# Kernel tuning notes

Hardware: AMD Instinct MI355X
Metric: run time of the kernel (lower is better)

Reference implementation:

```python
import jax, jax.numpy as jnp
import numpy as np

EMB = 768
HEADS = 8
HEAD_DIM = EMB // HEADS
SCALE = HEAD_DIM ** -0.5


def setup_inputs() -> dict:
    key = jax.random.key(0)
    ks = jax.random.split(key, 9)
    s = 0.02
    return {
        "x": jax.random.normal(ks[0], (2, 4096, EMB), dtype=jnp.float32),
        "Wq": jax.random.normal(ks[1], (EMB, EMB), dtype=jnp.float32) * s,
        "bq": jax.random.normal(ks[2], (EMB,), dtype=jnp.float32) * s,
        "Wk": jax.random.normal(ks[3], (EMB, EMB), dtype=jnp.float32) * s,
        "bk": jax.random.normal(ks[4], (EMB,), dtype=jnp.float32) * s,
        "Wv": jax.random.normal(ks[5], (EMB, EMB), dtype=jnp.float32) * s,
        "bv": jax.random.normal(ks[6], (EMB,), dtype=jnp.float32) * s,
        "Wo": jax.random.normal(ks[7], (EMB, EMB), dtype=jnp.float32) * s,
        "bo": jax.random.normal(ks[8], (EMB,), dtype=jnp.float32) * s,
    }


def reference(x, Wq, bq, Wk, bk, Wv, bv, Wo, bo):
    b, n, _ = x.shape
    # torch Linear: y = x @ W.T + b
    def split_heads(y):  # [b, n, emb] -> [b, h, n, d]
        return y.reshape(b, n, HEADS, HEAD_DIM).transpose(0, 2, 1, 3)

    q = split_heads(x @ Wq.T + bq)
    k = split_heads(x @ Wk.T + bk)
    v = split_heads(x @ Wv.T + bv)
    # scores [b, h, q, k]; source applies scaling inside softmax input
    scores = jnp.einsum('bhqd,bhkd->bhqk', q, k) * SCALE
    weight = jax.nn.softmax(scores, axis=-1)
    out = jnp.einsum('bhqk,bhkd->bhqd', weight, v)
    out = out.transpose(0, 2, 1, 3).reshape(b, n, EMB)
    return out @ Wo.T + bo
```

## Files before the change

### kernel.cpp

```cpp
#include <hip/hip_runtime.h>


typedef __bf16 bf16;
typedef __attribute__((ext_vector_type(2))) float f32x2;
typedef __attribute__((ext_vector_type(4))) float f32x4;
typedef __attribute__((ext_vector_type(16))) float f32x16;
typedef __attribute__((ext_vector_type(8))) __bf16 bf16x8;
typedef __attribute__((ext_vector_type(4))) __bf16 bf16x4;
typedef __attribute__((ext_vector_type(4))) unsigned u32x4;

#define EMB 768
#define SEQ 4096
#define NB 2
#define NHEADS 8
#define HD 96
#define BHTOT (NB * NHEADS)
#define MTOT (NB * SEQ)
#define QSCALE 0.14724241052735512f

#define AS1 __attribute__((address_space(1)))
#define AS3 __attribute__((address_space(3)))

__global__ __launch_bounds__(256) void cast_f32_bf16(const float* __restrict__ in,
                                                     bf16* __restrict__ out) {
  const int i = (blockIdx.x * 256 + threadIdx.x) * 4;
  const f32x4 v = *reinterpret_cast<const f32x4*>(in + i);
  bf16x4 o;
  o[0] = (bf16)v[0]; o[1] = (bf16)v[1]; o[2] = (bf16)v[2]; o[3] = (bf16)v[3];
  *reinterpret_cast<bf16x4*>(out + i) = o;
}

__global__ __launch_bounds__(256) void cast_w4(const float* __restrict__ w0,
                                               const float* __restrict__ w1,
                                               const float* __restrict__ w2,
                                               const float* __restrict__ w3,
                                               bf16* __restrict__ o0,
                                               bf16* __restrict__ o1,
                                               bf16* __restrict__ o2,
                                               bf16* __restrict__ o3) {
  const float* w = (blockIdx.y == 0) ? w0 : (blockIdx.y == 1) ? w1 : (blockIdx.y == 2) ? w2 : w3;
  bf16* o = (blockIdx.y == 0) ? o0 : (blockIdx.y == 1) ? o1 : (blockIdx.y == 2) ? o2 : o3;
  const int i = (blockIdx.x * 256 + threadIdx.x) * 4;
  const f32x4 v = *reinterpret_cast<const f32x4*>(w + i);
  bf16x4 ob;
  ob[0] = (bf16)v[0]; ob[1] = (bf16)v[1]; ob[2] = (bf16)v[2]; ob[3] = (bf16)v[3];
  *reinterpret_cast<bf16x4*>(o + i) = ob;
}

template <int MODE>
__global__ __launch_bounds__(256) void gemm_bt(const bf16* __restrict__ A,
                                               const bf16* __restrict__ B,
                                               const float* __restrict__ b0,
                                               const float* __restrict__ b1,
                                               const float* __restrict__ b2,
                                               void* __restrict__ out,
                                               void* __restrict__ outK) {
  constexpr int K = EMB;
  __shared__ bf16 As[128 * 32];
  __shared__ bf16 Bs[128 * 32];
  const int tid = threadIdx.x;
  const int lane = tid & 63;
  const int wid = tid >> 6;
  const int wr = wid >> 1, wc = wid & 1;
  const int l15 = lane & 15, l4 = lane >> 4;
  const int rowBase = blockIdx.y * 128;
  const int colBase = blockIdx.x * 128;

  f32x4 acc[4][4] = {};

  for (int kt = 0; kt < K / 32; ++kt) {
    const int kb = kt * 32;
#pragma unroll
    for (int i = 0; i < 2; ++i) {
      const int c = (wid * 2 + i) * 64 + lane;
      const int row = c >> 2, cc = c & 3;
      const bf16* ga = A + (size_t)(rowBase + row) * K + kb + cc * 8;
      const bf16* gb = B + (size_t)(colBase + row) * K + kb + cc * 8;
      __builtin_amdgcn_global_load_lds(
          (const AS1 void*)ga,
          (AS3 void*)(As + (size_t)(wid * 2 + i) * 512), 16, 0, 0);
      __builtin_amdgcn_global_load_lds(
          (const AS1 void*)gb,
          (AS3 void*)(Bs + (size_t)(wid * 2 + i) * 512), 16, 0, 0);
    }
    __syncthreads();
    bf16x8 af[4], bfr[4];
#pragma unroll
    for (int t = 0; t < 4; ++t) {
      af[t]  = *reinterpret_cast<const bf16x8*>(As + (wr * 64 + t * 16 + l15) * 32 + l4 * 8);
      bfr[t] = *reinterpret_cast<const bf16x8*>(Bs + (wc * 64 + t * 16 + l15) * 32 + l4 * 8);
    }
#pragma unroll
    for (int mt = 0; mt < 4; ++mt)
#pragma unroll
      for (int nt = 0; nt < 4; ++nt)
        acc[mt][nt] = __builtin_amdgcn_mfma_f32_16x16x32_bf16(af[mt], bfr[nt], acc[mt][nt], 0, 0, 0);
    __syncthreads();
  }

#pragma unroll
  for (int mt = 0; mt < 4; ++mt) {
#pragma unroll
    for (int nt = 0; nt < 4; ++nt) {
      const int gn = colBase + wc * 64 + nt * 16 + l15;
      if (MODE == 0) {
        const int mm = gn / 768;
        const int g7 = gn - mm * 768;
        const int h = g7 / HD, d = g7 - h * HD;
        const float* bp = (mm == 0) ? b0 : (mm == 1) ? b1 : b2;
        const float bv = bp[g7];
        const float sc = (mm == 0) ? QSCALE : 1.f;
#pragma unroll
        for (int r = 0; r < 4; ++r) {
          const int gm = rowBase + wr * 64 + mt * 16 + l4 * 4 + r;
          const int b = gm >> 12, n = gm & (SEQ - 1);
          const float v = (acc[mt][nt][r] + bv) * sc;
          if (mm == 1) {
            ((bf16*)outK)[((size_t)(b * NHEADS + h) * SEQ + n) * 128 +
                          (((d >> 3) ^ (n & 7)) << 3) + (d & 7)] = (bf16)v;
          } else {
            bf16* dst = (bf16*)out + (mm == 2 ? (size_t)MTOT * EMB : 0);
            dst[((size_t)(b * NHEADS + h) * SEQ + n) * HD + d] = (bf16)v;
          }
        }
      } else {
        const float bv = b0[gn];
#pragma unroll
        for (int r = 0; r < 4; ++r) {
          const int gm = rowBase + wr * 64 + mt * 16 + l4 * 4 + r;
          ((float*)out)[(size_t)gm * EMB + gn] = acc[mt][nt][r] + bv;
        }
      }
    }
  }
}

__global__ __launch_bounds__(256) void transpose_v(const bf16* __restrict__ v,
                                                   bf16* __restrict__ vt) {
  __shared__ bf16 T[96][72];
  const int bh = blockIdx.y;
  const int n0 = blockIdx.x * 64;
  const int tid = threadIdx.x;
#pragma unroll
  for (int i = 0; i < 3; ++i) {
    const int c = i * 256 + tid;
    const int n = c / 12, cc = c % 12;
    const bf16x8 val = *reinterpret_cast<const bf16x8*>(
        v + ((size_t)bh * SEQ + n0 + n) * HD + cc * 8);
#pragma unroll
    for (int j = 0; j < 8; ++j) T[cc * 8 + j][n] = val[j];
  }
  __syncthreads();
#pragma unroll
  for (int i = 0; i < 3; ++i) {
    const int c = i * 256 + tid;
    const int d = c >> 3, nc = c & 7;
    const int s0i = (nc >> 1) * 16 + (nc & 1) * 4;
    const bf16x4 lo = *reinterpret_cast<const bf16x4*>(&T[d][s0i]);
    const bf16x4 hi = *reinterpret_cast<const bf16x4*>(&T[d][s0i + 8]);
    const bf16x8 val = __builtin_shufflevector(lo, hi, 0, 1, 2, 3, 4, 5, 6, 7);
    const int pc = nc ^ (d & 7);
    *reinterpret_cast<bf16x8*>(vt + ((size_t)bh * HD + d) * SEQ + n0 + pc * 8) = val;
  }
}

template <int SPLIT>
__global__ __launch_bounds__(256, 2) void attn_fwd(const bf16* __restrict__ q,
                                                   const bf16* __restrict__ ksw,
                                                   const bf16* __restrict__ vt,
                                                   void* __restrict__ outp,
                                                   float* __restrict__ lsum) {
  __shared__ bf16 Ks[2][64 * 128];
  __shared__ bf16 Vts[2][96 * 64];
  const int tid = threadIdx.x;
  const int lane = tid & 63;
  const int wid = tid >> 6;
  const int l31 = lane & 31, lhi = lane >> 5;
  const int lin = (blockIdx.z * gridDim.y + blockIdx.y) * gridDim.x + blockIdx.x;
  const int nblk = 256 * SPLIT;
  const int cpx = nblk >> 3;
  const int l2 = (lin & 7) * cpx + (lin >> 3);
  const int qblk = l2 & 15;
  const int z = (SPLIT == 2) ? ((l2 >> 4) & 1) : 0;
  const int bh = (SPLIT == 2) ? (l2 >> 5) : (l2 >> 4);
  const int q0 = qblk * 256 + wid * 64;
  constexpr int NT = SEQ / 64 / SPLIT;
  const int kv00 = z * NT * 64;
  const size_t headq = (size_t)bh * SEQ * HD;
  const bf16* kg = ksw + (size_t)bh * SEQ * 128;
  const bf16* vg = vt + (size_t)bh * (size_t)HD * SEQ;

  const bf16* kp = kg + (size_t)kv00 * 128 + (size_t)tid * 8;
  const bf16* vp = vg + (size_t)(tid >> 3) * SEQ + kv00 + (tid & 7) * 8;

  int krd[12], vrd[12];
#pragma unroll
  for (int kib = 0; kib < 2; ++kib)
#pragma unroll
    for (int dc = 0; dc < 6; ++dc) {
      const int row = kib * 32 + l31;
      krd[kib * 6 + dc] = (row * 128 + (((dc * 2 + lhi) ^ (l31 & 7)) * 8)) * 2;
    }
#pragma unroll
  for (int db = 0; db < 3; ++db)
#pragma unroll
    for (int kb = 0; kb < 4; ++kb) {
      const int row = db * 32 + l31;
      vrd[db * 4 + kb] = (row * 64 + (((kb * 2 + lhi) ^ (l31 & 7)) * 8)) * 2;
    }

  bf16x8 qf[2][6];
#pragma unroll
  for (int g = 0; g < 2; ++g)
#pragma unroll
    for (int dc = 0; dc < 6; ++dc)
      qf[g][dc] = *reinterpret_cast<const bf16x8*>(
          q + headq + (size_t)(q0 + g * 32 + l31) * HD + dc * 16 + lhi * 8);

  f32x16 oacc[2][3] = {};
  float lrun[2] = {0.f, 0.f};

#pragma unroll
  for (int i = 0; i < 4; ++i)
    __builtin_amdgcn_global_load_lds((const AS1 void*)(kp + i * 2048),
                                     (AS3 void*)(&Ks[0][i * 2048 + tid * 8]), 16, 0, 0);
#pragma unroll
  for (int i = 0; i < 3; ++i)
    __builtin_amdgcn_global_load_lds((const AS1 void*)(vp + (size_t)i * 32 * SEQ),
                                     (AS3 void*)(&Vts[0][i * 2048 + tid * 8]), 16, 0, 0);
  kp += 8192;
  vp += 64;
  __syncthreads();

  for (int kt = 0; kt < NT; ++kt) {
    const int cur = kt & 1;
    if (kt < NT - 1) {
#pragma unroll
      for (int i = 0; i < 4; ++i)
        __builtin_amdgcn_global_load_lds((const AS1 void*)(kp + i * 2048),
                                         (AS3 void*)(&Ks[cur ^ 1][i * 2048 + tid * 8]), 16, 0, 0);
#pragma unroll
      for (int i = 0; i < 3; ++i)
        __builtin_amdgcn_global_load_lds((const AS1 void*)(vp + (size_t)i * 32 * SEQ),
                                         (AS3 void*)(&Vts[cur ^ 1][i * 2048 + tid * 8]), 16, 0, 0);
      kp += 8192;
      vp += 64;
    }
    const char* ksb = (const char*)Ks[cur];
    const char* vsb = (const char*)Vts[cur];

    bf16x8 pf[2][4];
#pragma unroll
    for (int kib = 0; kib < 2; ++kib) {
      f32x16 s[2] = {};
      __builtin_amdgcn_s_setprio(1);
#pragma unroll
      for (int dc = 0; dc < 6; ++dc) {
        const bf16x8 kf = *reinterpret_cast<const bf16x8*>(ksb + krd[kib * 6 + dc]);
        s[0] = __builtin_amdgcn_mfma_f32_32x32x16_bf16(kf, qf[0][dc], s[0], 0, 0, 0);
        s[1] = __builtin_amdgcn_mfma_f32_32x32x16_bf16(kf, qf[1][dc], s[1], 0, 0, 0);
      }
      __builtin_amdgcn_s_setprio(0);
#pragma unroll
      for (int g = 0; g < 2; ++g) {
        float a0 = 0.f, a1 = 0.f, a2 = 0.f, a3 = 0.f;
#pragma unroll
        for (int i = 0; i < 4; ++i) {
          s[g][4 * i + 0] = __builtin_amdgcn_exp2f(s[g][4 * i + 0]); a0 += s[g][4 * i + 0];
          s[g][4 * i + 1] = __builtin_amdgcn_exp2f(s[g][4 * i + 1]); a1 += s[g][4 * i + 1];
          s[g][4 * i + 2] = __builtin_amdgcn_exp2f(s[g][4 * i + 2]); a2 += s[g][4 * i + 2];
          s[g][4 * i + 3] = __builtin_amdgcn_exp2f(s[g][4 * i + 3]); a3 += s[g][4 * i + 3];
        }
        lrun[g] += (a0 + a1) + (a2 + a3);
        unsigned c[8];
#pragma unroll
        for (int i = 0; i < 8; ++i)
          asm("v_cvt_pk_bf16_f32 %0, %1, %2"
              : "=v"(c[i]) : "v"(s[g][2 * i]), "v"(s[g][2 * i + 1]));
        const u32x4 wa = {c[0], c[1], c[2], c[3]};
        const u32x4 wb = {c[4], c[5], c[6], c[7]};
        pf[g][kib * 2 + 0] = __builtin_bit_cast(bf16x8, wa);
        pf[g][kib * 2 + 1] = __builtin_bit_cast(bf16x8, wb);
      }
    }

    __builtin_amdgcn_s_setprio(1);
#pragma unroll
    for (int kb = 0; kb < 4; ++kb) {
#pragma unroll
      for (int db = 0; db < 3; ++db) {
        const bf16x8 vf = *reinterpret_cast<const bf16x8*>(vsb + vrd[db * 4 + kb]);
        oacc[0][db] = __builtin_amdgcn_mfma_f32_32x32x16_bf16(vf, pf[0][kb], oacc[0][db], 0, 0, 0);
        oacc[1][db] = __builtin_amdgcn_mfma_f32_32x32x16_bf16(vf, pf[1][kb], oacc[1][db], 0, 0, 0);
      }
    }
    __builtin_amdgcn_s_setprio(0);

    __syncthreads();
  }

  const int b = bh >> 3, h = bh & 7;
#pragma unroll
  for (int g = 0; g < 2; ++g) {
    float lr = lrun[g];
    lr += __shfl_xor(lr, 32, 64);
    const int n = q0 + g * 32 + l31;
    if (SPLIT == 2) {
      float* po = (float*)outp + (size_t)z * ((size_t)BHTOT * SEQ * HD) +
                  ((size_t)bh * SEQ + n) * HD;
#pragma unroll
      for (int db = 0; db < 3; ++db)
#pragma unroll
        for (int i = 0; i < 8; ++i) {
          const int r = 2 * i;
          const int d = db * 32 + (r & 3) + 8 * (r >> 2) + 4 * lhi;
          f32x2 w = {oacc[g][db][r], oacc[g][db][r + 1]};
          *reinterpret_cast<f32x2*>(po + d) = w;
        }
      if (lhi == 0) lsum[(size_t)z * BHTOT * SEQ + (size_t)bh * SEQ + n] = lr;
    } else {
      const float inv = 1.f / lr;
      bf16* obase = (bf16*)outp + (size_t)(b * SEQ + n) * EMB + h * HD;
#pragma unroll
      for (int db = 0; db < 3; ++db)
#pragma unroll
        for (int i = 0; i < 8; ++i) {
          const int r = 2 * i;
          const int d = db * 32 + (r & 3) + 8 * (r >> 2) + 4 * lhi;
          unsigned w;
          const float v0 = oacc[g][db][r] * inv, v1 = oacc[g][db][r + 1] * inv;
          asm("v_cvt_pk_bf16_f32 %0, %1, %2" : "=v"(w) : "v"(v0), "v"(v1));
          *reinterpret_cast<unsigned*>(obase + d) = w;
        }
    }
  }
}

__global__ __launch_bounds__(256) void merge_o(const float* __restrict__ p,
                                               const float* __restrict__ ls,
                                               bf16* __restrict__ ao) {
  const int idx = blockIdx.x * 256 + threadIdx.x;
  const size_t PS = (size_t)BHTOT * SEQ * HD;
  const f32x4 a = *reinterpret_cast<const f32x4*>(p + (size_t)idx * 4);
  const f32x4 b2 = *reinterpret_cast<const f32x4*>(p + PS + (size_t)idx * 4);
  const int rest = idx / 24;
  const int d4 = idx - rest * 24;
  const float inv = 1.f / (ls[rest] + ls[BHTOT * SEQ + rest]);
  const int bh = rest >> 12, n = rest & (SEQ - 1);
  const int b = bh >> 3, h = bh & 7;
  bf16x4 o4;
#pragma unroll
  for (int j = 0; j < 4; ++j) o4[j] = (bf16)((a[j] + b2[j]) * inv);
  *reinterpret_cast<bf16x4*>(ao + (size_t)(b * SEQ + n) * EMB + h * HD + d4 * 4) = o4;
}

extern "C" void kernel_launch(void* const* d_in, const int* in_sizes, int n_in,
                              void* d_out, int out_size, void* d_ws, size_t ws_size,
                              hipStream_t stream) {
  const float* x  = (const float*)d_in[0];
  const float* Wq = (const float*)d_in[1];
  const float* bq = (const float*)d_in[2];
  const float* Wk = (const float*)d_in[3];
  const float* bk = (const float*)d_in[4];
  const float* Wv = (const float*)d_in[5];
  const float* bv = (const float*)d_in[6];
  const float* Wo = (const float*)d_in[7];
  const float* bo = (const float*)d_in[8];

  const size_t XN = (size_t)MTOT * EMB;
  const size_t WN = (size_t)EMB * EMB;
  const size_t KSWN = (size_t)BHTOT * SEQ * 128;

  bf16* p = (bf16*)d_ws;
  bf16* xbf  = p; p += XN;
  bf16* wqb  = p; p += WN;
  bf16* wkb  = p; p += WN;
  bf16* wvb  = p; p += WN;
  bf16* wob  = p; p += WN;
  bf16* qb   = p; p += XN;
  bf16* vb   = p; p += XN;
  bf16* kbsw = p; p += KSWN;
  bf16* vtb  = p; p += XN;
  bf16* ao   = p; p += XN;
  const size_t base_bytes = (size_t)((char*)p - (char*)d_ws);
  float* part = (float*)p;
  float* lsum = part + 2 * ((size_t)BHTOT * SEQ * HD);
  const size_t need2 = base_bytes + (2 * (size_t)BHTOT * SEQ * HD) * 4 +
                       (2 * (size_t)BHTOT * SEQ) * 4;
  const bool split2 = (ws_size >= need2);

  cast_f32_bf16<<<XN / 1024, 256, 0, stream>>>(x, xbf);
  cast_w4<<<dim3(WN / 1024, 4), 256, 0, stream>>>(Wq, Wk, Wv, Wo, wqb, wkb, wvb, wob);

  gemm_bt<0><<<dim3(3 * EMB / 128, MTOT / 128), 256, 0, stream>>>(
      xbf, wqb, bq, bk, bv, qb, kbsw);

  transpose_v<<<dim3(SEQ / 64, BHTOT), 256, 0, stream>>>(vb, vtb);

  if (split2) {
    attn_fwd<2><<<dim3(16, 16, 2), 256, 0, stream>>>(qb, kbsw, vtb, part, lsum);
    merge_o<<<(BHTOT * SEQ * HD / 4) / 256, 256, 0, stream>>>(part, lsum, ao);
  } else {
    attn_fwd<1><<<dim3(16, 16, 1), 256, 0, stream>>>(qb, kbsw, vtb, ao, nullptr);
  }

  gemm_bt<1><<<dim3(EMB / 128, MTOT / 128), 256, 0, stream>>>(
      ao, wob, bo, nullptr, nullptr, d_out, nullptr);
}
```

Measured before the change: 211.0 us.

## Halve attention query tile, compact unpadded K layout, bf16 split partials

```diff
diff --git a/kernel.cpp b/kernel.cpp
--- a/kernel.cpp
+++ b/kernel.cpp
@@ -2,7 +2,6 @@
 
 
 typedef __bf16 bf16;
-typedef __attribute__((ext_vector_type(2))) float f32x2;
 typedef __attribute__((ext_vector_type(4))) float f32x4;
 typedef __attribute__((ext_vector_type(16))) float f32x16;
 typedef __attribute__((ext_vector_type(8))) __bf16 bf16x8;
@@ -17,6 +16,7 @@
 #define BHTOT (NB * NHEADS)
 #define MTOT (NB * SEQ)
 #define QSCALE 0.14724241052735512f
+#define KIMG_BH (SEQ * 96)
 
 #define AS1 __attribute__((address_space(1)))
 #define AS3 __attribute__((address_space(3)))
@@ -116,8 +116,10 @@
           const int b = gm >> 12, n = gm & (SEQ - 1);
           const float v = (acc[mt][nt][r] + bv) * sc;
           if (mm == 1) {
-            ((bf16*)outK)[((size_t)(b * NHEADS + h) * SEQ + n) * 128 +
-                          (((d >> 3) ^ (n & 7)) << 3) + (d & 7)] = (bf16)v;
+            ((bf16*)outK)[(size_t)(b * NHEADS + h) * KIMG_BH +
+                          (size_t)(n >> 6) * 6144 + (d >> 5) * 2048 +
+                          (n & 63) * 32 +
+                          ((((d >> 3) & 3) ^ ((n >> 1) & 3)) << 3) + (d & 7)] = (bf16)v;
           } else {
             bf16* dst = (bf16*)out + (mm == 2 ? (size_t)MTOT * EMB : 0);
             dst[((size_t)(b * NHEADS + h) * SEQ + n) * HD + d] = (bf16)v;
@@ -165,32 +167,32 @@
 }
 
 template <int SPLIT>
-__global__ __launch_bounds__(256, 2) void attn_fwd(const bf16* __restrict__ q,
-                                                   const bf16* __restrict__ ksw,
+__global__ __launch_bounds__(256, 3) void attn_fwd(const bf16* __restrict__ q,
+                                                   const bf16* __restrict__ kimg,
                                                    const bf16* __restrict__ vt,
                                                    void* __restrict__ outp,
                                                    float* __restrict__ lsum) {
-  __shared__ bf16 Ks[2][64 * 128];
+  __shared__ bf16 Ks[2][3 * 2048];
   __shared__ bf16 Vts[2][96 * 64];
   const int tid = threadIdx.x;
   const int lane = tid & 63;
   const int wid = tid >> 6;
   const int l31 = lane & 31, lhi = lane >> 5;
   const int lin = (blockIdx.z * gridDim.y + blockIdx.y) * gridDim.x + blockIdx.x;
-  const int nblk = 256 * SPLIT;
-  const int cpx = nblk >> 3;
-  const int l2 = (lin & 7) * cpx + (lin >> 3);
-  const int qblk = l2 & 15;
-  const int z = (SPLIT == 2) ? ((l2 >> 4) & 1) : 0;
-  const int bh = (SPLIT == 2) ? (l2 >> 5) : (l2 >> 4);
-  const int q0 = qblk * 256 + wid * 64;
+  constexpr int NBLK = 512 * SPLIT;
+  constexpr int CPX = NBLK >> 3;
+  const int l2 = (lin & 7) * CPX + (lin >> 3);
+  const int qblk = l2 & 31;
+  const int z = (SPLIT == 2) ? ((l2 >> 5) & 1) : 0;
+  const int bh = (SPLIT == 2) ? (l2 >> 6) : (l2 >> 5);
+  const int q0 = qblk * 128 + wid * 32;
   constexpr int NT = SEQ / 64 / SPLIT;
   const int kv00 = z * NT * 64;
   const size_t headq = (size_t)bh * SEQ * HD;
-  const bf16* kg = ksw + (size_t)bh * SEQ * 128;
+  const bf16* kg = kimg + (size_t)bh * KIMG_BH;
   const bf16* vg = vt + (size_t)bh * (size_t)HD * SEQ;
 
-  const bf16* kp = kg + (size_t)kv00 * 128 + (size_t)tid * 8;
+  const bf16* kp = kg + (size_t)(kv00 >> 6) * 6144 + (size_t)tid * 8;
   const bf16* vp = vg + (size_t)(tid >> 3) * SEQ + kv00 + (tid & 7) * 8;
 
   int krd[12], vrd[12];
@@ -198,8 +200,10 @@
   for (int kib = 0; kib < 2; ++kib)
 #pragma unroll
     for (int dc = 0; dc < 6; ++dc) {
+      const int j = dc * 2 + lhi;
       const int row = kib * 32 + l31;
-      krd[kib * 6 + dc] = (row * 128 + (((dc * 2 + lhi) ^ (l31 & 7)) * 8)) * 2;
+      krd[kib * 6 + dc] =
+          ((j >> 2) * 2048 + row * 32 + (((j & 3) ^ ((l31 >> 1) & 3)) << 3)) * 2;
     }
 #pragma unroll
   for (int db = 0; db < 3; ++db)
@@ -209,26 +213,23 @@
       vrd[db * 4 + kb] = (row * 64 + (((kb * 2 + lhi) ^ (l31 & 7)) * 8)) * 2;
     }
 
-  bf16x8 qf[2][6];
-#pragma unroll
-  for (int g = 0; g < 2; ++g)
-#pragma unroll
-    for (int dc = 0; dc < 6; ++dc)
-      qf[g][dc] = *reinterpret_cast<const bf16x8*>(
-          q + headq + (size_t)(q0 + g * 32 + l31) * HD + dc * 16 + lhi * 8);
-
-  f32x16 oacc[2][3] = {};
-  float lrun[2] = {0.f, 0.f};
-
-#pragma unroll
-  for (int i = 0; i < 4; ++i)
+  bf16x8 qf[6];
+#pragma unroll
+  for (int dc = 0; dc < 6; ++dc)
+    qf[dc] = *reinterpret_cast<const bf16x8*>(
+        q + headq + (size_t)(q0 + l31) * HD + dc * 16 + lhi * 8);
+
+  f32x16 oacc[3] = {};
+  float lrun = 0.f;
+
+#pragma unroll
+  for (int i = 0; i < 3; ++i) {
     __builtin_amdgcn_global_load_lds((const AS1 void*)(kp + i * 2048),
                                      (AS3 void*)(&Ks[0][i * 2048 + tid * 8]), 16, 0, 0);
-#pragma unroll
-  for (int i = 0; i < 3; ++i)
     __builtin_amdgcn_global_load_lds((const AS1 void*)(vp + (size_t)i * 32 * SEQ),
                                      (AS3 void*)(&Vts[0][i * 2048 + tid * 8]), 16, 0, 0);
-  kp += 8192;
+  }
+  kp += 6144;
   vp += 64;
   __syncthreads();
 
@@ -236,52 +237,59 @@
     const int cur = kt & 1;
     if (kt < NT - 1) {
 #pragma unroll
-      for (int i = 0; i < 4; ++i)
+      for (int i = 0; i < 3; ++i) {
         __builtin_amdgcn_global_load_lds((const AS1 void*)(kp + i * 2048),
                                          (AS3 void*)(&Ks[cur ^ 1][i * 2048 + tid * 8]), 16, 0, 0);
-#pragma unroll
-      for (int i = 0; i < 3; ++i)
         __builtin_amdgcn_global_load_lds((const AS1 void*)(vp + (size_t)i * 32 * SEQ),
                                          (AS3 void*)(&Vts[cur ^ 1][i * 2048 + tid * 8]), 16, 0, 0);
-      kp += 8192;
+      }
+      kp += 6144;
       vp += 64;
     }
     const char* ksb = (const char*)Ks[cur];
     const char* vsb = (const char*)Vts[cur];
 
-    bf16x8 pf[2][4];
-#pragma unroll
-    for (int kib = 0; kib < 2; ++kib) {
-      f32x16 s[2] = {};
-      __builtin_amdgcn_s_setprio(1);
-#pragma unroll
-      for (int dc = 0; dc < 6; ++dc) {
-        const bf16x8 kf = *reinterpret_cast<const bf16x8*>(ksb + krd[kib * 6 + dc]);
-        s[0] = __builtin_amdgcn_mfma_f32_32x32x16_bf16(kf, qf[0][dc], s[0], 0, 0, 0);
-        s[1] = __builtin_amdgcn_mfma_f32_32x32x16_bf16(kf, qf[1][dc], s[1], 0, 0, 0);
-      }
-      __builtin_amdgcn_s_setprio(0);
-#pragma unroll
-      for (int g = 0; g < 2; ++g) {
-        float a0 = 0.f, a1 = 0.f, a2 = 0.f, a3 = 0.f;
-#pragma unroll
-        for (int i = 0; i < 4; ++i) {
-          s[g][4 * i + 0] = __builtin_amdgcn_exp2f(s[g][4 * i + 0]); a0 += s[g][4 * i + 0];
-          s[g][4 * i + 1] = __builtin_amdgcn_exp2f(s[g][4 * i + 1]); a1 += s[g][4 * i + 1];
-          s[g][4 * i + 2] = __builtin_amdgcn_exp2f(s[g][4 * i + 2]); a2 += s[g][4 * i + 2];
-          s[g][4 * i + 3] = __builtin_amdgcn_exp2f(s[g][4 * i + 3]); a3 += s[g][4 * i + 3];
-        }
-        lrun[g] += (a0 + a1) + (a2 + a3);
-        unsigned c[8];
-#pragma unroll
-        for (int i = 0; i < 8; ++i)
-          asm("v_cvt_pk_bf16_f32 %0, %1, %2"
-              : "=v"(c[i]) : "v"(s[g][2 * i]), "v"(s[g][2 * i + 1]));
-        const u32x4 wa = {c[0], c[1], c[2], c[3]};
-        const u32x4 wb = {c[4], c[5], c[6], c[7]};
-        pf[g][kib * 2 + 0] = __builtin_bit_cast(bf16x8, wa);
-        pf[g][kib * 2 + 1] = __builtin_bit_cast(bf16x8, wb);
-      }
+    f32x16 s0 = {}, s1 = {};
+    __builtin_amdgcn_s_setprio(1);
+#pragma unroll
+    for (int dc = 0; dc < 6; ++dc) {
+      const bf16x8 kf0 = *reinterpret_cast<const bf16x8*>(ksb + krd[dc]);
+      const bf16x8 kf1 = *reinterpret_cast<const bf16x8*>(ksb + krd[6 + dc]);
+      s0 = __builtin_amdgcn_mfma_f32_32x32x16_bf16(kf0, qf[dc], s0, 0, 0, 0);
+      s1 = __builtin_amdgcn_mfma_f32_32x32x16_bf16(kf1, qf[dc], s1, 0, 0, 0);
+    }
+    __builtin_amdgcn_s_setprio(0);
+
+    float a0 = 0.f, a1 = 0.f, a2 = 0.f, a3 = 0.f;
+#pragma unroll
+    for (int i = 0; i < 4; ++i) {
+      s0[4 * i + 0] = __builtin_amdgcn_exp2f(s0[4 * i + 0]); a0 += s0[4 * i + 0];
+      s0[4 * i + 1] = __builtin_amdgcn_exp2f(s0[4 * i + 1]); a1 += s0[4 * i + 1];
+      s0[4 * i + 2] = __builtin_amdgcn_exp2f(s0[4 * i + 2]); a2 += s0[4 * i + 2];
+      s0[4 * i + 3] = __builtin_amdgcn_exp2f(s0[4 * i + 3]); a3 += s0[4 * i + 3];
+    }
+#pragma unroll
+    for (int i = 0; i < 4; ++i) {
+      s1[4 * i + 0] = __builtin_amdgcn_exp2f(s1[4 * i + 0]); a0 += s1[4 * i + 0];
+      s1[4 * i + 1] = __builtin_amdgcn_exp2f(s1[4 * i + 1]); a1 += s1[4 * i + 1];
+      s1[4 * i + 2] = __builtin_amdgcn_exp2f(s1[4 * i + 2]); a2 += s1[4 * i + 2];
+      s1[4 * i + 3] = __builtin_amdgcn_exp2f(s1[4 * i + 3]); a3 += s1[4 * i + 3];
+    }
+    lrun += (a0 + a1) + (a2 + a3);
+
+    bf16x8 pf[4];
+#pragma unroll
+    for (int blk = 0; blk < 2; ++blk) {
+      const f32x16& s = blk ? s1 : s0;
+      unsigned c[8];
+#pragma unroll
+      for (int i = 0; i < 8; ++i)
+        asm("v_cvt_pk_bf16_f32 %0, %1, %2"
+            : "=v"(c[i]) : "v"(s[2 * i]), "v"(s[2 * i + 1]));
+      const u32x4 wa = {c[0], c[1], c[2], c[3]};
+      const u32x4 wb = {c[4], c[5], c[6], c[7]};
+      pf[blk * 2 + 0] = __builtin_bit_cast(bf16x8, wa);
+      pf[blk * 2 + 1] = __builtin_bit_cast(bf16x8, wb);
     }
 
     __builtin_amdgcn_s_setprio(1);
@@ -290,8 +298,7 @@
 #pragma unroll
       for (int db = 0; db < 3; ++db) {
         const bf16x8 vf = *reinterpret_cast<const bf16x8*>(vsb + vrd[db * 4 + kb]);
-        oacc[0][db] = __builtin_amdgcn_mfma_f32_32x32x16_bf16(vf, pf[0][kb], oacc[0][db], 0, 0, 0);
-        oacc[1][db] = __builtin_amdgcn_mfma_f32_32x32x16_bf16(vf, pf[1][kb], oacc[1][db], 0, 0, 0);
+        oacc[db] = __builtin_amdgcn_mfma_f32_32x32x16_bf16(vf, pf[kb], oacc[db], 0, 0, 0);
       }
     }
     __builtin_amdgcn_s_setprio(0);
@@ -299,59 +306,57 @@
     __syncthreads();
   }
 
+  lrun += __shfl_xor(lrun, 32, 64);
+  const int n = q0 + l31;
   const int b = bh >> 3, h = bh & 7;
-#pragma unroll
-  for (int g = 0; g < 2; ++g) {
-    float lr = lrun[g];
-    lr += __shfl_xor(lr, 32, 64);
-    const int n = q0 + g * 32 + l31;
-    if (SPLIT == 2) {
-      float* po = (float*)outp + (size_t)z * ((size_t)BHTOT * SEQ * HD) +
-                  ((size_t)bh * SEQ + n) * HD;
-#pragma unroll
-      for (int db = 0; db < 3; ++db)
-#pragma unroll
-        for (int i = 0; i < 8; ++i) {
-          const int r = 2 * i;
-          const int d = db * 32 + (r & 3) + 8 * (r >> 2) + 4 * lhi;
-          f32x2 w = {oacc[g][db][r], oacc[g][db][r + 1]};
-          *reinterpret_cast<f32x2*>(po + d) = w;
-        }
-      if (lhi == 0) lsum[(size_t)z * BHTOT * SEQ + (size_t)bh * SEQ + n] = lr;
-    } else {
-      const float inv = 1.f / lr;
-      bf16* obase = (bf16*)outp + (size_t)(b * SEQ + n) * EMB + h * HD;
-#pragma unroll
-      for (int db = 0; db < 3; ++db)
-#pragma unroll
-        for (int i = 0; i < 8; ++i) {
-          const int r = 2 * i;
-          const int d = db * 32 + (r & 3) + 8 * (r >> 2) + 4 * lhi;
-          unsigned w;
-          const float v0 = oacc[g][db][r] * inv, v1 = oacc[g][db][r + 1] * inv;
-          asm("v_cvt_pk_bf16_f32 %0, %1, %2" : "=v"(w) : "v"(v0), "v"(v1));
-          *reinterpret_cast<unsigned*>(obase + d) = w;
-        }
-    }
-  }
-}
-
-__global__ __launch_bounds__(256) void merge_o(const float* __restrict__ p,
+  if (SPLIT == 2) {
+    bf16* po = (bf16*)outp + (size_t)z * ((size_t)BHTOT * SEQ * HD) +
+               ((size_t)bh * SEQ + n) * HD;
+#pragma unroll
+    for (int db = 0; db < 3; ++db)
+#pragma unroll
+      for (int i = 0; i < 8; ++i) {
+        const int r = 2 * i;
+        const int d = db * 32 + (r & 3) + 8 * (r >> 2) + 4 * lhi;
+        unsigned w;
+        asm("v_cvt_pk_bf16_f32 %0, %1, %2"
+            : "=v"(w) : "v"(oacc[db][r]), "v"(oacc[db][r + 1]));
+        *reinterpret_cast<unsigned*>(po + d) = w;
+      }
+    if (lhi == 0) lsum[(size_t)z * BHTOT * SEQ + (size_t)bh * SEQ + n] = lrun;
+  } else {
+    const float inv = 1.f / lrun;
+    bf16* obase = (bf16*)outp + (size_t)(b * SEQ + n) * EMB + h * HD;
+#pragma unroll
+    for (int db = 0; db < 3; ++db)
+#pragma unroll
+      for (int i = 0; i < 8; ++i) {
+        const int r = 2 * i;
+        const int d = db * 32 + (r & 3) + 8 * (r >> 2) + 4 * lhi;
+        unsigned w;
+        const float v0 = oacc[db][r] * inv, v1 = oacc[db][r + 1] * inv;
+        asm("v_cvt_pk_bf16_f32 %0, %1, %2" : "=v"(w) : "v"(v0), "v"(v1));
+        *reinterpret_cast<unsigned*>(obase + d) = w;
+      }
+  }
+}
+
+__global__ __launch_bounds__(256) void merge_o(const bf16* __restrict__ p,
                                                const float* __restrict__ ls,
                                                bf16* __restrict__ ao) {
   const int idx = blockIdx.x * 256 + threadIdx.x;
   const size_t PS = (size_t)BHTOT * SEQ * HD;
-  const f32x4 a = *reinterpret_cast<const f32x4*>(p + (size_t)idx * 4);
-  const f32x4 b2 = *reinterpret_cast<const f32x4*>(p + PS + (size_t)idx * 4);
-  const int rest = idx / 24;
-  const int d4 = idx - rest * 24;
+  const int rest = idx / 12;
+  const int d8 = idx - rest * 12;
+  const bf16x8 a = *reinterpret_cast<const bf16x8*>(p + (size_t)idx * 8);
+  const bf16x8 b2 = *reinterpret_cast<const bf16x8*>(p + PS + (size_t)idx * 8);
   const float inv = 1.f / (ls[rest] + ls[BHTOT * SEQ + rest]);
   const int bh = rest >> 12, n = rest & (SEQ - 1);
   const int b = bh >> 3, h = bh & 7;
-  bf16x4 o4;
-#pragma unroll
-  for (int j = 0; j < 4; ++j) o4[j] = (bf16)((a[j] + b2[j]) * inv);
-  *reinterpret_cast<bf16x4*>(ao + (size_t)(b * SEQ + n) * EMB + h * HD + d4 * 4) = o4;
+  bf16x8 o8;
+#pragma unroll
+  for (int j = 0; j < 8; ++j) o8[j] = (bf16)(((float)a[j] + (float)b2[j]) * inv);
+  *reinterpret_cast<bf16x8*>(ao + (size_t)(b * SEQ + n) * EMB + h * HD + d8 * 8) = o8;
 }
 
 extern "C" void kernel_launch(void* const* d_in, const int* in_sizes, int n_in,
@@ -369,7 +374,7 @@
 
   const size_t XN = (size_t)MTOT * EMB;
   const size_t WN = (size_t)EMB * EMB;
-  const size_t KSWN = (size_t)BHTOT * SEQ * 128;
+  const size_t KSWN = (size_t)BHTOT * KIMG_BH;
 
   bf16* p = (bf16*)d_ws;
   bf16* xbf  = p; p += XN;
@@ -383,10 +388,10 @@
   bf16* vtb  = p; p += XN;
   bf16* ao   = p; p += XN;
   const size_t base_bytes = (size_t)((char*)p - (char*)d_ws);
-  float* part = (float*)p;
-  float* lsum = part + 2 * ((size_t)BHTOT * SEQ * HD);
-  const size_t need2 = base_bytes + (2 * (size_t)BHTOT * SEQ * HD) * 4 +
-                       (2 * (size_t)BHTOT * SEQ) * 4;
+  const size_t PS = (size_t)BHTOT * SEQ * HD;
+  bf16* part = p;
+  float* lsum = (float*)(p + 2 * PS);
+  const size_t need2 = base_bytes + 2 * PS * 2 + 2 * (size_t)BHTOT * SEQ * 4;
   const bool split2 = (ws_size >= need2);
 
   cast_f32_bf16<<<XN / 1024, 256, 0, stream>>>(x, xbf);
@@ -398,10 +403,10 @@
   transpose_v<<<dim3(SEQ / 64, BHTOT), 256, 0, stream>>>(vb, vtb);
 
   if (split2) {
-    attn_fwd<2><<<dim3(16, 16, 2), 256, 0, stream>>>(qb, kbsw, vtb, part, lsum);
-    merge_o<<<(BHTOT * SEQ * HD / 4) / 256, 256, 0, stream>>>(part, lsum, ao);
+    attn_fwd<2><<<dim3(32, 16, 2), 256, 0, stream>>>(qb, kbsw, vtb, part, lsum);
+    merge_o<<<(int)(PS / 8 / 256), 256, 0, stream>>>(part, lsum, ao);
   } else {
-    attn_fwd<1><<<dim3(16, 16, 1), 256, 0, stream>>>(qb, kbsw, vtb, ao, nullptr);
+    attn_fwd<1><<<dim3(32, 16, 1), 256, 0, stream>>>(qb, kbsw, vtb, ao, nullptr);
   }
 
   gemm_bt<1><<<dim3(EMB / 128, MTOT / 128), 256, 0, stream>>>(
```

Measured after the change: 220.8 us. 4.6% more time.
